# Optimization experiments

Hardware: AMD Instinct MI355X
Metric: run time of the kernel (lower is better)

## Reference

```python
import jax, jax.numpy as jnp
import numpy as np

N_NODES = 50000
N_EDGES = 800000
IN_HID = 64
OUT_HID = 64
EXT_DIM = 32


def setup_inputs() -> dict:
    key = jax.random.key(0)
    ks = jax.random.split(key, 9)
    h = jax.random.normal(ks[0], (N_NODES, IN_HID), dtype=jnp.float32)
    e_h = jax.random.normal(ks[1], (N_EDGES, IN_HID), dtype=jnp.float32)
    ext_feature = jax.random.normal(ks[2], (N_EDGES, EXT_DIM), dtype=jnp.float32)
    # fc1: Linear(3*in_hid -> in_hid); fc2: Linear(in_hid+ext_dim -> out_hid)
    W1 = jax.random.normal(ks[3], (3 * IN_HID, IN_HID), dtype=jnp.float32) * 0.05
    b1 = jax.random.normal(ks[4], (IN_HID,), dtype=jnp.float32) * 0.05
    W2 = jax.random.normal(ks[5], (IN_HID + EXT_DIM, OUT_HID), dtype=jnp.float32) * 0.05
    b2 = jax.random.normal(ks[6], (OUT_HID,), dtype=jnp.float32) * 0.05
    src = jax.random.randint(ks[7], (N_EDGES,), 0, N_NODES, dtype=jnp.int64 if jax.config.jax_enable_x64 else jnp.int32)
    dst = jax.random.randint(ks[8], (N_EDGES,), 0, N_NODES, dtype=jnp.int64 if jax.config.jax_enable_x64 else jnp.int32)
    return {"h": h, "e_h": e_h, "ext_feature": ext_feature,
            "W1": W1, "b1": b1, "W2": W2, "b2": b2,
            "src": src, "dst": dst}


def reference(h, e_h, ext_feature, W1, b1, W2, b2, src, dst):
    # apply_edge: gather src/dst node features, concat with edge feature
    evt = jnp.concatenate([h[src], e_h, h[dst]], axis=-1)          # [E, 3*in_hid]
    x = evt @ W1 + b1                                              # fc1 (dropout=0 -> identity)
    x = jnp.concatenate([x, ext_feature], axis=-1)                 # [E, in_hid+ext_dim]
    out = jax.nn.relu(x @ W2 + b2)                                 # fc2 + relu; activation=None
    return out                                                     # new edge feature e_h [E, out_hid]
```

## Files before the change

kernel.cpp:

```cpp
#include <hip/hip_runtime.h>


typedef __attribute__((ext_vector_type(8))) short bf16x8;
typedef __attribute__((ext_vector_type(4))) float f32x4;

__device__ __forceinline__ short f2bf(float f) {
  unsigned u = __builtin_bit_cast(unsigned, f);
  u = (u + 0x7FFFu + ((u >> 16) & 1u)) >> 16;
  return (short)u;
}


__global__ __launch_bounds__(256, 2) void edge_mp_kernel(
    const float* __restrict__ h, const float* __restrict__ e_h,
    const float* __restrict__ ext, const float* __restrict__ W1,
    const float* __restrict__ b1, const float* __restrict__ W2,
    const float* __restrict__ b2, const int* __restrict__ src,
    const int* __restrict__ dst, float* __restrict__ out, int E) {
  __shared__ __align__(16) short lds[30720];
  const int tid = threadIdx.x;
  const int l = tid & 63;
  const int wid = tid >> 6;
  const int i = l & 15;
  const int q = l >> 4;
  const int i2 = l >> 2;
  const int c = l & 3;

  for (int s = tid; s < 1536; s += 256) {
    int kc = s >> 8, nt = (s >> 6) & 3, ll = s & 63;
    int k0 = kc * 32 + ((ll >> 4) * 8), n = nt * 16 + (ll & 15);
#pragma unroll
    for (int j = 0; j < 8; ++j) lds[s * 8 + j] = f2bf(W1[(k0 + j) * 64 + n]);
  }
  for (int s = tid; s < 768; s += 256) {
    int kc = s >> 8, nt = (s >> 6) & 3, ll = s & 63;
    int k0 = kc * 32 + ((ll >> 4) * 8), n = nt * 16 + (ll & 15);
#pragma unroll
    for (int j = 0; j < 8; ++j)
      lds[12288 + s * 8 + j] = f2bf(W2[(k0 + j) * 64 + n]);
  }
  __syncthreads();

  float b1v[4], b2v[4];
#pragma unroll
  for (int nt = 0; nt < 4; ++nt) {
    b1v[nt] = b1[nt * 16 + i];
    b2v[nt] = b2[nt * 16 + i];
  }

  short* evt = &lds[18432 + wid * 3072];

  for (int it = 0; it < 4; ++it) {
    const int e0 = blockIdx.x * 256 + it * 64 + wid * 16;
    if (e0 >= E) break;
    int e = e0 + i2;
    if (e >= E) e = E - 1;
    const int sI = src[e], dI = dst[e];
    const float* srcp[3] = {h + (size_t)sI * 64, e_h + (size_t)e * 64,
                            h + (size_t)dI * 64};

#pragma unroll
    for (int s = 0; s < 3; ++s) {
#pragma unroll
      for (int t = 0; t < 4; ++t) {
        const int k0 = 16 * t + 4 * c;
        float4 v = *(const float4*)(srcp[s] + k0);
        const int kc = s * 2 + (t >> 1);
        const int quad = 2 * (t & 1) + (c >> 1);
        const int j0 = 4 * (c & 1);
        short4 p;
        p.x = f2bf(v.x); p.y = f2bf(v.y); p.z = f2bf(v.z); p.w = f2bf(v.w);
        *(short4*)&evt[(kc * 64 + quad * 16 + i2) * 8 + j0] = p;
      }
    }

    f32x4 acc[4] = {{0.f, 0.f, 0.f, 0.f},
                    {0.f, 0.f, 0.f, 0.f},
                    {0.f, 0.f, 0.f, 0.f},
                    {0.f, 0.f, 0.f, 0.f}};
#pragma unroll
    for (int kc = 0; kc < 6; ++kc) {
      bf16x8 a = *(const bf16x8*)&evt[(kc * 64 + l) * 8];
#pragma unroll
      for (int nt = 0; nt < 4; ++nt) {
        bf16x8 b = *(const bf16x8*)&lds[((kc * 4 + nt) * 64 + l) * 8];
        acc[nt] = __builtin_amdgcn_mfma_f32_16x16x32_bf16(a, b, acc[nt], 0, 0, 0);
      }
    }

#pragma unroll
    for (int nt = 0; nt < 4; ++nt) {
      const int n = nt * 16 + i;
      const int kc2 = n >> 5, qA = (n & 31) >> 3, j = n & 7;
#pragma unroll
      for (int r = 0; r < 4; ++r) {
        const int m = q * 4 + r;
        evt[(kc2 * 64 + qA * 16 + m) * 8 + j] = f2bf(acc[nt][r] + b1v[nt]);
      }
    }
#pragma unroll
    for (int t = 0; t < 2; ++t) {
      float4 v = *(const float4*)(ext + (size_t)e * 32 + 16 * t + 4 * c);
      const int quad = 2 * t + (c >> 1);
      const int j0 = 4 * (c & 1);
      short4 p;
      p.x = f2bf(v.x); p.y = f2bf(v.y); p.z = f2bf(v.z); p.w = f2bf(v.w);
      *(short4*)&evt[(2 * 64 + quad * 16 + i2) * 8 + j0] = p;
    }

    f32x4 acc2[4] = {{0.f, 0.f, 0.f, 0.f},
                     {0.f, 0.f, 0.f, 0.f},
                     {0.f, 0.f, 0.f, 0.f},
                     {0.f, 0.f, 0.f, 0.f}};
#pragma unroll
    for (int kc = 0; kc < 3; ++kc) {
      bf16x8 a = *(const bf16x8*)&evt[(kc * 64 + l) * 8];
#pragma unroll
      for (int nt = 0; nt < 4; ++nt) {
        bf16x8 b = *(const bf16x8*)&lds[12288 + ((kc * 4 + nt) * 64 + l) * 8];
        acc2[nt] =
            __builtin_amdgcn_mfma_f32_16x16x32_bf16(a, b, acc2[nt], 0, 0, 0);
      }
    }

#pragma unroll
    for (int nt = 0; nt < 4; ++nt) {
      const int n = nt * 16 + i;
#pragma unroll
      for (int r = 0; r < 4; ++r) {
        const int er = e0 + q * 4 + r;
        if (er < E) {
          float v = acc2[nt][r] + b2v[nt];
          out[(size_t)er * 64 + n] = fmaxf(v, 0.f);
        }
      }
    }
  }
}

extern "C" void kernel_launch(void* const* d_in, const int* in_sizes, int n_in,
                              void* d_out, int out_size, void* d_ws,
                              size_t ws_size, hipStream_t stream) {
  const float* h = (const float*)d_in[0];
  const float* e_h = (const float*)d_in[1];
  const float* ext = (const float*)d_in[2];
  const float* W1 = (const float*)d_in[3];
  const float* b1 = (const float*)d_in[4];
  const float* W2 = (const float*)d_in[5];
  const float* b2 = (const float*)d_in[6];
  const int* src = (const int*)d_in[7];
  const int* dst = (const int*)d_in[8];
  float* out = (float*)d_out;
  const int E = in_sizes[7];
  const int blocks = (E + 255) / 256;
  hipLaunchKernelGGL(edge_mp_kernel, dim3(blocks), dim3(256), 0, stream, h, e_h,
                     ext, W1, b1, W2, b2, src, dst, out, E);
}
```

Measured before the change: 457.1 us.

## Load MFMA A-operands directly from global into registers, bypassing LDS staging

```diff
diff --git a/kernel.cpp b/kernel.cpp
--- a/kernel.cpp
+++ b/kernel.cpp
@@ -10,34 +10,42 @@
   return (short)u;
 }
 
+__device__ __forceinline__ bf16x8 pack8(float4 a, float4 b) {
+  bf16x8 r;
+  r[0] = f2bf(a.x); r[1] = f2bf(a.y); r[2] = f2bf(a.z); r[3] = f2bf(a.w);
+  r[4] = f2bf(b.x); r[5] = f2bf(b.y); r[6] = f2bf(b.z); r[7] = f2bf(b.w);
+  return r;
+}
 
-__global__ __launch_bounds__(256, 2) void edge_mp_kernel(
+
+__global__ __launch_bounds__(256, 3) void edge_mp_kernel(
     const float* __restrict__ h, const float* __restrict__ e_h,
     const float* __restrict__ ext, const float* __restrict__ W1,
     const float* __restrict__ b1, const float* __restrict__ W2,
     const float* __restrict__ b2, const int* __restrict__ src,
     const int* __restrict__ dst, float* __restrict__ out, int E) {
-  __shared__ __align__(16) short lds[30720];
+  __shared__ __align__(16) short lds[22528];
   const int tid = threadIdx.x;
   const int l = tid & 63;
   const int wid = tid >> 6;
   const int i = l & 15;
   const int q = l >> 4;
-  const int i2 = l >> 2;
-  const int c = l & 3;
 
   for (int s = tid; s < 1536; s += 256) {
     int kc = s >> 8, nt = (s >> 6) & 3, ll = s & 63;
     int k0 = kc * 32 + ((ll >> 4) * 8), n = nt * 16 + (ll & 15);
+    bf16x8 w;
 #pragma unroll
-    for (int j = 0; j < 8; ++j) lds[s * 8 + j] = f2bf(W1[(k0 + j) * 64 + n]);
+    for (int j = 0; j < 8; ++j) w[j] = f2bf(W1[(k0 + j) * 64 + n]);
+    *(bf16x8*)&lds[s * 8] = w;
   }
   for (int s = tid; s < 768; s += 256) {
     int kc = s >> 8, nt = (s >> 6) & 3, ll = s & 63;
     int k0 = kc * 32 + ((ll >> 4) * 8), n = nt * 16 + (ll & 15);
+    bf16x8 w;
 #pragma unroll
-    for (int j = 0; j < 8; ++j)
-      lds[12288 + s * 8 + j] = f2bf(W2[(k0 + j) * 64 + n]);
+    for (int j = 0; j < 8; ++j) w[j] = f2bf(W2[(k0 + j) * 64 + n]);
+    *(bf16x8*)&lds[12288 + s * 8] = w;
   }
   __syncthreads();
 
@@ -48,39 +56,44 @@
     b2v[nt] = b2[nt * 16 + i];
   }
 
-  short* evt = &lds[18432 + wid * 3072];
+  short* xb = &lds[18432 + wid * 1024];
+
+  int e_nxt = blockIdx.x * 256 + wid * 16 + i;
+  if (e_nxt >= E) e_nxt = E - 1;
+  int sI_nxt = src[e_nxt], dI_nxt = dst[e_nxt];
 
   for (int it = 0; it < 4; ++it) {
     const int e0 = blockIdx.x * 256 + it * 64 + wid * 16;
     if (e0 >= E) break;
-    int e = e0 + i2;
-    if (e >= E) e = E - 1;
-    const int sI = src[e], dI = dst[e];
-    const float* srcp[3] = {h + (size_t)sI * 64, e_h + (size_t)e * 64,
-                            h + (size_t)dI * 64};
-
-#pragma unroll
-    for (int s = 0; s < 3; ++s) {
-#pragma unroll
-      for (int t = 0; t < 4; ++t) {
-        const int k0 = 16 * t + 4 * c;
-        float4 v = *(const float4*)(srcp[s] + k0);
-        const int kc = s * 2 + (t >> 1);
-        const int quad = 2 * (t & 1) + (c >> 1);
-        const int j0 = 4 * (c & 1);
-        short4 p;
-        p.x = f2bf(v.x); p.y = f2bf(v.y); p.z = f2bf(v.z); p.w = f2bf(v.w);
-        *(short4*)&evt[(kc * 64 + quad * 16 + i2) * 8 + j0] = p;
-      }
+    const int e = e_nxt;
+    const int sI = sI_nxt, dI = dI_nxt;
+    if (it < 3) {
+      int en = e0 + 64 + i;
+      if (en >= E) en = E - 1;
+      e_nxt = en;
+      sI_nxt = src[en];
+      dI_nxt = dst[en];
     }
 
-    f32x4 acc[4] = {{0.f, 0.f, 0.f, 0.f},
-                    {0.f, 0.f, 0.f, 0.f},
-                    {0.f, 0.f, 0.f, 0.f},
-                    {0.f, 0.f, 0.f, 0.f}};
+    const float* ps = h + (size_t)sI * 64 + q * 8;
+    const float* pe = e_h + (size_t)e * 64 + q * 8;
+    const float* pd = h + (size_t)dI * 64 + q * 8;
+    const float* px = ext + (size_t)e * 32 + q * 8;
+    float4 ld[12];
+    ld[0] = *(const float4*)(ps);      ld[1] = *(const float4*)(ps + 4);
+    ld[2] = *(const float4*)(ps + 32); ld[3] = *(const float4*)(ps + 36);
+    ld[4] = *(const float4*)(pe);      ld[5] = *(const float4*)(pe + 4);
+    ld[6] = *(const float4*)(pe + 32); ld[7] = *(const float4*)(pe + 36);
+    ld[8] = *(const float4*)(pd);      ld[9] = *(const float4*)(pd + 4);
+    ld[10] = *(const float4*)(pd + 32); ld[11] = *(const float4*)(pd + 36);
+    float4 x0 = *(const float4*)(px);
+    float4 x1 = *(const float4*)(px + 4);
+
+    f32x4 acc[4] = {{0.f, 0.f, 0.f, 0.f}, {0.f, 0.f, 0.f, 0.f},
+                    {0.f, 0.f, 0.f, 0.f}, {0.f, 0.f, 0.f, 0.f}};
 #pragma unroll
     for (int kc = 0; kc < 6; ++kc) {
-      bf16x8 a = *(const bf16x8*)&evt[(kc * 64 + l) * 8];
+      bf16x8 a = pack8(ld[kc * 2], ld[kc * 2 + 1]);
 #pragma unroll
       for (int nt = 0; nt < 4; ++nt) {
         bf16x8 b = *(const bf16x8*)&lds[((kc * 4 + nt) * 64 + l) * 8];
@@ -91,33 +104,31 @@
 #pragma unroll
     for (int nt = 0; nt < 4; ++nt) {
       const int n = nt * 16 + i;
-      const int kc2 = n >> 5, qA = (n & 31) >> 3, j = n & 7;
+      const int slotbase = (n >> 5) * 64 + ((n & 31) >> 3) * 16;
+      const int j = n & 7;
 #pragma unroll
       for (int r = 0; r < 4; ++r) {
-        const int m = q * 4 + r;
-        evt[(kc2 * 64 + qA * 16 + m) * 8 + j] = f2bf(acc[nt][r] + b1v[nt]);
+        xb[(slotbase + q * 4 + r) * 8 + j] = f2bf(acc[nt][r] + b1v[nt]);
       }
     }
+
+    f32x4 acc2[4] = {{0.f, 0.f, 0.f, 0.f}, {0.f, 0.f, 0.f, 0.f},
+                     {0.f, 0.f, 0.f, 0.f}, {0.f, 0.f, 0.f, 0.f}};
 #pragma unroll
-    for (int t = 0; t < 2; ++t) {
-      float4 v = *(const float4*)(ext + (size_t)e * 32 + 16 * t + 4 * c);
-      const int quad = 2 * t + (c >> 1);
-      const int j0 = 4 * (c & 1);
-      short4 p;
-      p.x = f2bf(v.x); p.y = f2bf(v.y); p.z = f2bf(v.z); p.w = f2bf(v.w);
-      *(short4*)&evt[(2 * 64 + quad * 16 + i2) * 8 + j0] = p;
-    }
-
-    f32x4 acc2[4] = {{0.f, 0.f, 0.f, 0.f},
-                     {0.f, 0.f, 0.f, 0.f},
-                     {0.f, 0.f, 0.f, 0.f},
-                     {0.f, 0.f, 0.f, 0.f}};
-#pragma unroll
-    for (int kc = 0; kc < 3; ++kc) {
-      bf16x8 a = *(const bf16x8*)&evt[(kc * 64 + l) * 8];
+    for (int kc = 0; kc < 2; ++kc) {
+      bf16x8 a = *(const bf16x8*)&xb[(kc * 64 + l) * 8];
 #pragma unroll
       for (int nt = 0; nt < 4; ++nt) {
         bf16x8 b = *(const bf16x8*)&lds[12288 + ((kc * 4 + nt) * 64 + l) * 8];
+        acc2[nt] =
+            __builtin_amdgcn_mfma_f32_16x16x32_bf16(a, b, acc2[nt], 0, 0, 0);
+      }
+    }
+    {
+      bf16x8 a = pack8(x0, x1);
+#pragma unroll
+      for (int nt = 0; nt < 4; ++nt) {
+        bf16x8 b = *(const bf16x8*)&lds[12288 + ((2 * 4 + nt) * 64 + l) * 8];
         acc2[nt] =
             __builtin_amdgcn_mfma_f32_16x16x32_bf16(a, b, acc2[nt], 0, 0, 0);
       }
@@ -130,8 +141,7 @@
       for (int r = 0; r < 4; ++r) {
         const int er = e0 + q * 4 + r;
         if (er < E) {
-          float v = acc2[nt][r] + b2v[nt];
-          out[(size_t)er * 64 + n] = fmaxf(v, 0.f);
+          out[(size_t)er * 64 + n] = fmaxf(acc2[nt][r] + b2v[nt], 0.f);
         }
       }
     }
```

Result: slower. 475.7 us (+4.1%).
